# Optimization experiments

Hardware: AMD Instinct MI355X
Metric: run time of the kernel (lower is better)

The kernel has to match this reference:

```python
import jax, jax.numpy as jnp
import numpy as np

N_HEAD = 16
MASK_NEG = 1e10  # matches torch's -10000000000.0 * (1 - b)


def setup_inputs() -> dict:
    key = jax.random.key(0)
    ks = jax.random.split(key, 9)
    B, S, D = 2, 2048, 2048
    std = 0.02
    inp = {
        "x": jax.random.normal(ks[0], (B, S, D), dtype=jnp.float32),
        "Wq": jax.random.normal(ks[1], (D, D), dtype=jnp.float32) * std,
        "bq": jnp.zeros((D,), dtype=jnp.float32),
        "Wk": jax.random.normal(ks[2], (D, D), dtype=jnp.float32) * std,
        "bk": jnp.zeros((D,), dtype=jnp.float32),
        "Wv": jax.random.normal(ks[3], (D, D), dtype=jnp.float32) * std,
        "bv": jnp.zeros((D,), dtype=jnp.float32),
        "Wd": jax.random.normal(ks[4], (D, D), dtype=jnp.float32) * std,
        "bd": jnp.zeros((D,), dtype=jnp.float32),
    }
    return inp


def reference(x, Wq, bq, Wk, bk, Wv, bv, Wd, bd):
    # x: [B, S, D]; layer_past=None, query=None path (full causal prefill)
    B, S, D = x.shape
    H = N_HEAD
    hd = D // H

    def split(h):  # [B,S,D] -> [B,H,S,hd]
        return h.reshape(B, S, H, hd).transpose(0, 2, 1, 3)

    q = split(x @ Wq + bq)
    k = split(x @ Wk + bk)
    v = split(x @ Wv + bv)

    # scores [B,H,S,S]; scale=True divides by sqrt(head_dim)
    w = jnp.einsum("bhqd,bhkd->bhqk", q, k) / jnp.sqrt(jnp.float32(hd))
    b = jnp.tril(jnp.ones((S, S), dtype=w.dtype))  # causal bias buffer slice
    w = w * b - MASK_NEG * (1.0 - b)
    w = jax.nn.softmax(w, axis=-1)
    a = jnp.einsum("bhqk,bhkd->bhqd", w, v)

    a = a.transpose(0, 2, 1, 3).reshape(B, S, D)  # merge_heads
    a = a @ Wd + bd
    present = jnp.stack((k, v))  # [2, B, H, S, hd]
    return a, present
```

## Files before the change

### kernel.cpp

```cpp
#include <hip/hip_runtime.h>


typedef unsigned short ushort_t;
typedef __attribute__((ext_vector_type(8))) short short8;
typedef __attribute__((ext_vector_type(4))) float f32x4;

#define MFMA16x16x32 __builtin_amdgcn_mfma_f32_16x16x32_bf16
#define S_LEN   2048
#define DMODEL  2048
#define A_ELEMS 8388608
#define W_ELEMS 4194304

__device__ __forceinline__ ushort_t f2bf(float x) {
  unsigned u = __float_as_uint(x);
  u += 0x7FFFu + ((u >> 16) & 1u);
  return (ushort_t)(u >> 16);
}
__device__ __forceinline__ unsigned pack2(float lo, float hi) {
  return (unsigned)f2bf(lo) | ((unsigned)f2bf(hi) << 16);
}
struct f8 { float v[8]; };
__device__ __forceinline__ f8 ld8f(const float* p) {
  f8 r;
  float4 a = *(const float4*)p, b = *(const float4*)(p + 4);
  r.v[0]=a.x; r.v[1]=a.y; r.v[2]=a.z; r.v[3]=a.w;
  r.v[4]=b.x; r.v[5]=b.y; r.v[6]=b.z; r.v[7]=b.w;
  return r;
}
__device__ __forceinline__ uint4 cvt8(const f8& f) {
  uint4 o;
  o.x = pack2(f.v[0], f.v[1]); o.y = pack2(f.v[2], f.v[3]);
  o.z = pack2(f.v[4], f.v[5]); o.w = pack2(f.v[6], f.v[7]);
  return o;
}

typedef const __attribute__((address_space(1))) void* gas_t;
typedef __attribute__((address_space(3))) void* las_t;
__device__ __forceinline__ void gld16(const void* g, void* l) {
  __builtin_amdgcn_global_load_lds((gas_t)(unsigned long long)g,
                                   (las_t)(unsigned)(unsigned long long)l,
                                   16, 0, 0);
}

__global__ void __launch_bounds__(256) conv_x(const float* __restrict__ x,
                                              ushort_t* __restrict__ xb) {
  const int i = (blockIdx.x * 256 + threadIdx.x) * 8;
  f8 v = ld8f(x + i);
  *(uint4*)&xb[i] = cvt8(v);
}

__global__ void __launch_bounds__(256) trans_w(
    const float* __restrict__ w0, const float* __restrict__ w1,
    const float* __restrict__ w2, const float* __restrict__ w3,
    ushort_t* __restrict__ o0, ushort_t* __restrict__ o1,
    ushort_t* __restrict__ o2, ushort_t* __restrict__ o3) {
  __shared__ float t[64][65];
  const float* src; ushort_t* dst;
  switch (blockIdx.z) {
    case 0: src = w0; dst = o0; break;
    case 1: src = w1; dst = o1; break;
    case 2: src = w2; dst = o2; break;
    default: src = w3; dst = o3; break;
  }
  const int kb = blockIdx.y * 64, nb = blockIdx.x * 64;
  const int r = threadIdx.x >> 3, c8 = (threadIdx.x & 7) * 8;
#pragma unroll
  for (int i = 0; i < 64; i += 32) {
    *(float4*)&t[r + i][c8]     = *(const float4*)&src[(size_t)(kb + r + i) * DMODEL + nb + c8];
    *(float4*)&t[r + i][c8 + 4] = *(const float4*)&src[(size_t)(kb + r + i) * DMODEL + nb + c8 + 4];
  }
  __syncthreads();
#pragma unroll
  for (int i = 0; i < 64; i += 32) {
    float tmp[8];
#pragma unroll
    for (int j = 0; j < 8; ++j) tmp[j] = t[c8 + j][r + i];
    uint4 o;
    o.x = pack2(tmp[0], tmp[1]); o.y = pack2(tmp[2], tmp[3]);
    o.z = pack2(tmp[4], tmp[5]); o.w = pack2(tmp[6], tmp[7]);
    *(uint4*)&dst[(size_t)(nb + r + i) * DMODEL + kb + c8] = o;
  }
}

__device__ __forceinline__ void gemm_core(
    const ushort_t* __restrict__ gA, const ushort_t* __restrict__ gB,
    ushort_t* As, ushort_t* Bs, int w, int lane, int wr, int wc,
    f32x4 acc[4][4]) {
  const int sr = lane >> 2, sc = (lane & 3) * 8;
  const int l15 = lane & 15, quad = lane >> 4;
  const ushort_t* pA = gA + sc;
  const ushort_t* pB = gB + sc;
  for (int kt = 0; kt < 2048; kt += 32) {
    __syncthreads();
#pragma unroll
    for (int i = 0; i < 4; ++i) {
      const int c = i * 4 + w;
      if (c < 8)
        gld16(pA + (size_t)(c * 16 + sr) * 2048 + kt, (void*)(As + c * 512));
      else
        gld16(pB + (size_t)((c - 8) * 16 + sr) * 2048 + kt,
              (void*)(Bs + (c - 8) * 512));
    }
    __syncthreads();
    short8 af[4], bf[4];
#pragma unroll
    for (int mi = 0; mi < 4; ++mi)
      af[mi] = *(const short8*)&As[(wr + mi * 16 + l15) * 32 + quad * 8];
#pragma unroll
    for (int ni = 0; ni < 4; ++ni)
      bf[ni] = *(const short8*)&Bs[(wc + ni * 16 + l15) * 32 + quad * 8];
#pragma unroll
    for (int mi = 0; mi < 4; ++mi)
#pragma unroll
      for (int ni = 0; ni < 4; ++ni)
        acc[mi][ni] = MFMA16x16x32(af[mi], bf[ni], acc[mi][ni], 0, 0, 0);
  }
}

__global__ void __launch_bounds__(256) gemm_qkv(
    const ushort_t* __restrict__ xb,
    const ushort_t* __restrict__ wtq, const ushort_t* __restrict__ wtk,
    const ushort_t* __restrict__ wtv,
    const float* __restrict__ bq, const float* __restrict__ bk,
    const float* __restrict__ bv,
    ushort_t* __restrict__ qout, float* __restrict__ kout,
    float* __restrict__ vout) {
  __shared__ ushort_t As[4096], Bs[4096];
  const int tid = threadIdx.x, w = tid >> 6, lane = tid & 63;
  const int l15 = lane & 15, quad = lane >> 4;
  const int bx = blockIdx.x, wid = bx >> 9, r = bx & 511;
  const int tm = r & 31, tn = r >> 5;
  const int wr = (w >> 1) * 64, wc = (w & 1) * 64;
  const ushort_t* Wt = wid == 0 ? wtq : (wid == 1 ? wtk : wtv);
  const float* bias = wid == 0 ? bq : (wid == 1 ? bk : bv);

  f32x4 acc[4][4] = {};
  gemm_core(xb + (size_t)(tm * 128) * 2048, Wt + (size_t)(tn * 128) * 2048,
            As, Bs, w, lane, wr, wc, acc);

  const int row0 = tm * 128 + wr, col0 = tn * 128 + wc;
#pragma unroll
  for (int ni = 0; ni < 4; ++ni) {
    const int col = col0 + ni * 16 + l15;
    const float bv_ = bias[col];
    const int h = col >> 7, d = col & 127;
#pragma unroll
    for (int mi = 0; mi < 4; ++mi) {
#pragma unroll
      for (int j = 0; j < 4; ++j) {
        const int row = row0 + mi * 16 + quad * 4 + j;
        const int b = row >> 11, s = row & 2047;
        const size_t idx = (size_t)(((b * 16 + h) * 2048 + s)) * 128 + d;
        const float v = acc[mi][ni][j] + bv_;
        if (wid == 0) qout[idx] = f2bf(v);
        else if (wid == 1) kout[idx] = v;
        else vout[idx] = v;
      }
    }
  }
}

__global__ void __launch_bounds__(256) gemm_proj(
    const ushort_t* __restrict__ A, const ushort_t* __restrict__ Wt,
    const float* __restrict__ bias, float* __restrict__ C) {
  __shared__ ushort_t As[4096], Bs[4096];
  const int tid = threadIdx.x, w = tid >> 6, lane = tid & 63;
  const int l15 = lane & 15, quad = lane >> 4;
  const int tm = blockIdx.x & 31, tn = blockIdx.x >> 5;
  const int wr = (w >> 1) * 64, wc = (w & 1) * 64;

  f32x4 acc[4][4] = {};
  gemm_core(A + (size_t)(tm * 128) * 2048, Wt + (size_t)(tn * 128) * 2048,
            As, Bs, w, lane, wr, wc, acc);

  const int row0 = tm * 128 + wr, col0 = tn * 128 + wc;
#pragma unroll
  for (int ni = 0; ni < 4; ++ni) {
    const int col = col0 + ni * 16 + l15;
    const float bv_ = bias[col];
#pragma unroll
    for (int mi = 0; mi < 4; ++mi)
#pragma unroll
      for (int j = 0; j < 4; ++j) {
        const int row = row0 + mi * 16 + quad * 4 + j;
        C[(size_t)row * DMODEL + col] = acc[mi][ni][j] + bv_;
      }
  }
}

__global__ void __launch_bounds__(256) attn_fwd(
    const ushort_t* __restrict__ Q, const float* __restrict__ Kx,
    const float* __restrict__ Vx, ushort_t* __restrict__ O) {
  __shared__ ushort_t Ks[128 * 136];
  __shared__ ushort_t Vs[128 * 72];
  const int tid = threadIdx.x;
  const int w = tid >> 6, lane = tid & 63;
  const int l15 = lane & 15, quad = lane >> 4;
  const int bh = blockIdx.x & 31, pr = blockIdx.x >> 5;
  const int b = bh >> 4, h = bh & 15;
  const size_t base = (size_t)bh * (S_LEN * 128);
  const float cs = 0.08838834764831845f * 1.4426950408889634f;

  const int kr = tid >> 1, kc0 = (tid & 1) * 64;
  const int vk = (tid & 31) * 2, vo = (tid >> 5) * 16;

  for (int seg = 0; seg < 2; ++seg) {
    const int qt = (seg == 0) ? (15 - pr) : pr;
    const int q0 = qt * 128 + w * 32;

    short8 qf[2][4];
#pragma unroll
    for (int mi = 0; mi < 2; ++mi)
#pragma unroll
      for (int ks = 0; ks < 4; ++ks)
        qf[mi][ks] = *(const short8*)&Q[base +
            (size_t)(q0 + mi * 16 + l15) * 128 + ks * 32 + quad * 8];

    f32x4 oacc[2][8] = {};
    float mrun[2][4], lrun[2][4];
#pragma unroll
    for (int mi = 0; mi < 2; ++mi)
#pragma unroll
      for (int j = 0; j < 4; ++j) { mrun[mi][j] = -1e30f; lrun[mi][j] = 0.f; }

    for (int kt = 0; kt <= qt; ++kt) {
      const int kb = kt * 128;
      __syncthreads();
#pragma unroll
      for (int j = 0; j < 8; ++j) {
        f8 kk = ld8f(&Kx[base + (size_t)(kb + kr) * 128 + kc0 + j * 8]);
        *(uint4*)&Ks[kr * 136 + kc0 + j * 8] = cvt8(kk);
      }
      {
        f8 a0 = ld8f(&Vx[base + (size_t)(kb + vk) * 128 + vo]);
        f8 a1 = ld8f(&Vx[base + (size_t)(kb + vk) * 128 + vo + 8]);
        f8 b0 = ld8f(&Vx[base + (size_t)(kb + vk + 1) * 128 + vo]);
        f8 b1 = ld8f(&Vx[base + (size_t)(kb + vk + 1) * 128 + vo + 8]);
#pragma unroll
        for (int j = 0; j < 8; ++j) {
          *(unsigned*)&Vs[(vo + j) * 72 + vk]     = pack2(a0.v[j], b0.v[j]);
          *(unsigned*)&Vs[(vo + 8 + j) * 72 + vk] = pack2(a1.v[j], b1.v[j]);
        }
      }
      __syncthreads();

      f32x4 sacc[2][8] = {};
#pragma unroll
      for (int ks = 0; ks < 4; ++ks) {
        short8 kf[8];
#pragma unroll
        for (int ni = 0; ni < 8; ++ni)
          kf[ni] = *(const short8*)&Ks[(ni * 16 + l15) * 136 + ks * 32 + quad * 8];
#pragma unroll
        for (int mi = 0; mi < 2; ++mi)
#pragma unroll
          for (int ni = 0; ni < 8; ++ni)
            sacc[mi][ni] = MFMA16x16x32(qf[mi][ks], kf[ni], sacc[mi][ni], 0, 0, 0);
      }
      __syncthreads();

#pragma unroll
      for (int mi = 0; mi < 2; ++mi) {
#pragma unroll
        for (int j = 0; j < 4; ++j) {
          const int rl = mi * 16 + quad * 4 + j;
          const int rowg = q0 + rl;
          float t0[8];
#pragma unroll
          for (int ni = 0; ni < 8; ++ni) {
            const int kg = kb + ni * 16 + l15;
            const float s = sacc[mi][ni][j] * cs;
            t0[ni] = (kg <= rowg) ? s : -1e30f;
          }
          float rm = t0[0];
#pragma unroll
          for (int ni = 1; ni < 8; ++ni) rm = fmaxf(rm, t0[ni]);
          rm = fmaxf(rm, __shfl_xor(rm, 1));
          rm = fmaxf(rm, __shfl_xor(rm, 2));
          rm = fmaxf(rm, __shfl_xor(rm, 4));
          rm = fmaxf(rm, __shfl_xor(rm, 8));
          const float mold = mrun[mi][j];
          const float mnew = fmaxf(mold, rm);
          const float alpha = __builtin_amdgcn_exp2f(mold - mnew);
          float rs = 0.f;
#pragma unroll
          for (int ni = 0; ni < 8; ++ni) {
            const float pe = __builtin_amdgcn_exp2f(t0[ni] - mnew);
            rs += pe;
            Ks[(w * 32 + rl) * 136 + ni * 16 + l15] = f2bf(pe);
          }
          rs += __shfl_xor(rs, 1);
          rs += __shfl_xor(rs, 2);
          rs += __shfl_xor(rs, 4);
          rs += __shfl_xor(rs, 8);
          lrun[mi][j] = lrun[mi][j] * alpha + rs;
          mrun[mi][j] = mnew;
#pragma unroll
          for (int oi = 0; oi < 8; ++oi) oacc[mi][oi][j] *= alpha;
        }
      }

#pragma unroll
      for (int hh = 0; hh < 2; ++hh) {
        if (hh == 1) {
          __syncthreads();
          f8 a0 = ld8f(&Vx[base + (size_t)(kb + 64 + vk) * 128 + vo]);
          f8 a1 = ld8f(&Vx[base + (size_t)(kb + 64 + vk) * 128 + vo + 8]);
          f8 b0 = ld8f(&Vx[base + (size_t)(kb + 64 + vk + 1) * 128 + vo]);
          f8 b1 = ld8f(&Vx[base + (size_t)(kb + 64 + vk + 1) * 128 + vo + 8]);
#pragma unroll
          for (int j = 0; j < 8; ++j) {
            *(unsigned*)&Vs[(vo + j) * 72 + vk]     = pack2(a0.v[j], b0.v[j]);
            *(unsigned*)&Vs[(vo + 8 + j) * 72 + vk] = pack2(a1.v[j], b1.v[j]);
          }
          __syncthreads();
        }
#pragma unroll
        for (int ks = 0; ks < 2; ++ks) {
          short8 pf[2], vf[8];
#pragma unroll
          for (int mi = 0; mi < 2; ++mi)
            pf[mi] = *(const short8*)&Ks[(w * 32 + mi * 16 + l15) * 136 +
                                         hh * 64 + ks * 32 + quad * 8];
#pragma unroll
          for (int oi = 0; oi < 8; ++oi)
            vf[oi] = *(const short8*)&Vs[(oi * 16 + l15) * 72 + ks * 32 + quad * 8];
#pragma unroll
          for (int mi = 0; mi < 2; ++mi)
#pragma unroll
            for (int oi = 0; oi < 8; ++oi)
              oacc[mi][oi] = MFMA16x16x32(pf[mi], vf[oi], oacc[mi][oi], 0, 0, 0);
        }
      }
    }

#pragma unroll
    for (int mi = 0; mi < 2; ++mi) {
      float inv[4];
#pragma unroll
      for (int j = 0; j < 4; ++j) inv[j] = 1.f / lrun[mi][j];
#pragma unroll
      for (int oi = 0; oi < 8; ++oi) {
        const int oc = oi * 16 + l15;
#pragma unroll
        for (int j = 0; j < 4; ++j) {
          const int s = q0 + mi * 16 + quad * 4 + j;
          O[((size_t)(b * S_LEN + s)) * DMODEL + h * 128 + oc] =
              f2bf(oacc[mi][oi][j] * inv[j]);
        }
      }
    }
  }
}

extern "C" void kernel_launch(void* const* d_in, const int* in_sizes, int n_in,
                              void* d_out, int out_size, void* d_ws,
                              size_t ws_size, hipStream_t stream) {
  const float* x  = (const float*)d_in[0];
  const float* Wq = (const float*)d_in[1];
  const float* bq = (const float*)d_in[2];
  const float* Wk = (const float*)d_in[3];
  const float* bk = (const float*)d_in[4];
  const float* Wv = (const float*)d_in[5];
  const float* bv = (const float*)d_in[6];
  const float* Wd = (const float*)d_in[7];
  const float* bd = (const float*)d_in[8];

  float* out   = (float*)d_out;
  float* a_out = out;
  float* k_out = out + A_ELEMS;
  float* v_out = out + 2 * A_ELEMS;
  ushort_t* ob  = (ushort_t*)d_out;
  ushort_t* xb   = ob;
  ushort_t* q_ws = ob + A_ELEMS;

  ushort_t* ws  = (ushort_t*)d_ws;
  ushort_t* wtq = ws;
  ushort_t* wtk = ws + W_ELEMS;
  ushort_t* wtv = ws + 2 * (size_t)W_ELEMS;
  ushort_t* wtd = ws + 3 * (size_t)W_ELEMS;
  ushort_t* attn_ws = ws + 4 * (size_t)W_ELEMS;

  conv_x<<<4096, 256, 0, stream>>>(x, xb);
  trans_w<<<dim3(32, 32, 4), 256, 0, stream>>>(Wq, Wk, Wv, Wd,
                                               wtq, wtk, wtv, wtd);
  gemm_qkv<<<1536, 256, 0, stream>>>(xb, wtq, wtk, wtv, bq, bk, bv,
                                     q_ws, k_out, v_out);
  attn_fwd<<<256, 256, 0, stream>>>(q_ws, k_out, v_out, attn_ws);
  gemm_proj<<<512, 256, 0, stream>>>(attn_ws, wtd, bd, a_out);
}
```

Before: 523.7 us.

## Pre-convert K/V to bf16 with transposed V and async swizzled LDS loads in attention

The QKV GEMM now also writes a bf16 copy of K, and a new kernel transposes V into a bf16 [d][s] layout. The attention kernel loads both tiles straight into XOR-swizzled shared memory with direct global-to-LDS loads, replacing the per-tile fp32-to-bf16 conversion and the scalar V transpose. It also moves to 512 threads, with each wave owning 16 query rows, and loads the whole V tile at once instead of in two halves. This removes conversion work and extra syncs inside the inner loop, at the cost of an extra kernel, more workspace, and extra global writes for the bf16 K and transposed V copies.

```diff
diff --git a/kernel.cpp b/kernel.cpp
--- a/kernel.cpp
+++ b/kernel.cpp
@@ -82,6 +82,32 @@
   }
 }
 
+__global__ void __launch_bounds__(256) trans_v(const float* __restrict__ v,
+                                               ushort_t* __restrict__ vt) {
+  __shared__ float t[64][65];
+  const int bh = blockIdx.z;
+  const int sb = blockIdx.x * 64, db = blockIdx.y * 64;
+  const float* src = v + (size_t)bh * S_LEN * 128;
+  ushort_t* dst = vt + (size_t)bh * 128 * S_LEN;
+  const int r = threadIdx.x >> 3, c8 = (threadIdx.x & 7) * 8;
+#pragma unroll
+  for (int i = 0; i < 64; i += 32) {
+    *(float4*)&t[r + i][c8]     = *(const float4*)&src[(size_t)(sb + r + i) * 128 + db + c8];
+    *(float4*)&t[r + i][c8 + 4] = *(const float4*)&src[(size_t)(sb + r + i) * 128 + db + c8 + 4];
+  }
+  __syncthreads();
+#pragma unroll
+  for (int i = 0; i < 64; i += 32) {
+    float tmp[8];
+#pragma unroll
+    for (int j = 0; j < 8; ++j) tmp[j] = t[c8 + j][r + i];
+    uint4 o;
+    o.x = pack2(tmp[0], tmp[1]); o.y = pack2(tmp[2], tmp[3]);
+    o.z = pack2(tmp[4], tmp[5]); o.w = pack2(tmp[6], tmp[7]);
+    *(uint4*)&dst[(size_t)(db + r + i) * S_LEN + sb + c8] = o;
+  }
+}
+
 __device__ __forceinline__ void gemm_core(
     const ushort_t* __restrict__ gA, const ushort_t* __restrict__ gB,
     ushort_t* As, ushort_t* Bs, int w, int lane, int wr, int wc,
@@ -124,7 +150,7 @@
     const float* __restrict__ bq, const float* __restrict__ bk,
     const float* __restrict__ bv,
     ushort_t* __restrict__ qout, float* __restrict__ kout,
-    float* __restrict__ vout) {
+    float* __restrict__ vout, ushort_t* __restrict__ kb16) {
   __shared__ ushort_t As[4096], Bs[4096];
   const int tid = threadIdx.x, w = tid >> 6, lane = tid & 63;
   const int l15 = lane & 15, quad = lane >> 4;
@@ -153,7 +179,7 @@
         const size_t idx = (size_t)(((b * 16 + h) * 2048 + s)) * 128 + d;
         const float v = acc[mi][ni][j] + bv_;
         if (wid == 0) qout[idx] = f2bf(v);
-        else if (wid == 1) kout[idx] = v;
+        else if (wid == 1) { kout[idx] = v; kb16[idx] = f2bf(v); }
         else vout[idx] = v;
       }
     }
@@ -188,165 +214,129 @@
   }
 }
 
-__global__ void __launch_bounds__(256) attn_fwd(
-    const ushort_t* __restrict__ Q, const float* __restrict__ Kx,
-    const float* __restrict__ Vx, ushort_t* __restrict__ O) {
-  __shared__ ushort_t Ks[128 * 136];
-  __shared__ ushort_t Vs[128 * 72];
+__global__ void __launch_bounds__(512, 2) attn_fwd(
+    const ushort_t* __restrict__ Q, const ushort_t* __restrict__ Kb,
+    const ushort_t* __restrict__ Vt, ushort_t* __restrict__ O) {
+  __shared__ ushort_t KP[128 * 136];
+  __shared__ ushort_t Vs[128 * 128];
   const int tid = threadIdx.x;
   const int w = tid >> 6, lane = tid & 63;
   const int l15 = lane & 15, quad = lane >> 4;
+  const int x7 = l15 & 7;
   const int bh = blockIdx.x & 31, pr = blockIdx.x >> 5;
   const int b = bh >> 4, h = bh & 15;
-  const size_t base = (size_t)bh * (S_LEN * 128);
+  const size_t base  = (size_t)bh * (S_LEN * 128);
+  const size_t vbase = (size_t)bh * (128 * S_LEN);
   const float cs = 0.08838834764831845f * 1.4426950408889634f;
 
-  const int kr = tid >> 1, kc0 = (tid & 1) * 64;
-  const int vk = (tid & 31) * 2, vo = (tid >> 5) * 16;
+  const int srow = lane >> 4;
+  const int schunk = lane & 15;
 
   for (int seg = 0; seg < 2; ++seg) {
     const int qt = (seg == 0) ? (15 - pr) : pr;
-    const int q0 = qt * 128 + w * 32;
-
-    short8 qf[2][4];
-#pragma unroll
-    for (int mi = 0; mi < 2; ++mi)
-#pragma unroll
-      for (int ks = 0; ks < 4; ++ks)
-        qf[mi][ks] = *(const short8*)&Q[base +
-            (size_t)(q0 + mi * 16 + l15) * 128 + ks * 32 + quad * 8];
-
-    f32x4 oacc[2][8] = {};
-    float mrun[2][4], lrun[2][4];
-#pragma unroll
-    for (int mi = 0; mi < 2; ++mi)
-#pragma unroll
-      for (int j = 0; j < 4; ++j) { mrun[mi][j] = -1e30f; lrun[mi][j] = 0.f; }
+    const int q0 = qt * 128 + w * 16;
+
+    short8 qf[4];
+#pragma unroll
+    for (int ks = 0; ks < 4; ++ks)
+      qf[ks] = *(const short8*)&Q[base + (size_t)(q0 + l15) * 128 + ks * 32 + quad * 8];
+
+    f32x4 oacc[8] = {};
+    float mrun[4], lrun[4];
+#pragma unroll
+    for (int j = 0; j < 4; ++j) { mrun[j] = -1e30f; lrun[j] = 0.f; }
 
     for (int kt = 0; kt <= qt; ++kt) {
-      const int kb = kt * 128;
+      const int kb_ = kt * 128;
       __syncthreads();
 #pragma unroll
-      for (int j = 0; j < 8; ++j) {
-        f8 kk = ld8f(&Kx[base + (size_t)(kb + kr) * 128 + kc0 + j * 8]);
-        *(uint4*)&Ks[kr * 136 + kc0 + j * 8] = cvt8(kk);
-      }
-      {
-        f8 a0 = ld8f(&Vx[base + (size_t)(kb + vk) * 128 + vo]);
-        f8 a1 = ld8f(&Vx[base + (size_t)(kb + vk) * 128 + vo + 8]);
-        f8 b0 = ld8f(&Vx[base + (size_t)(kb + vk + 1) * 128 + vo]);
-        f8 b1 = ld8f(&Vx[base + (size_t)(kb + vk + 1) * 128 + vo + 8]);
-#pragma unroll
-        for (int j = 0; j < 8; ++j) {
-          *(unsigned*)&Vs[(vo + j) * 72 + vk]     = pack2(a0.v[j], b0.v[j]);
-          *(unsigned*)&Vs[(vo + 8 + j) * 72 + vk] = pack2(a1.v[j], b1.v[j]);
+      for (int i = 0; i < 4; ++i) {
+        const int r = w * 16 + i * 4 + srow;
+        const int c = schunk ^ (r & 7);
+        gld16(Kb + base + (size_t)(kb_ + r) * 128 + c * 8,
+              (void*)(KP + (w * 16 + i * 4) * 128));
+        gld16(Vt + vbase + (size_t)r * S_LEN + kb_ + c * 8,
+              (void*)(Vs + (w * 16 + i * 4) * 128));
+      }
+      __syncthreads();
+
+      f32x4 sacc[8] = {};
+#pragma unroll
+      for (int ks = 0; ks < 4; ++ks) {
+        const int sw = ((ks * 4 + quad) ^ x7) * 8;
+        short8 kf[8];
+#pragma unroll
+        for (int ni = 0; ni < 8; ++ni)
+          kf[ni] = *(const short8*)&KP[(ni * 16 + l15) * 128 + sw];
+#pragma unroll
+        for (int ni = 0; ni < 8; ++ni)
+          sacc[ni] = MFMA16x16x32(qf[ks], kf[ni], sacc[ni], 0, 0, 0);
+      }
+      __syncthreads();
+
+#pragma unroll
+      for (int j = 0; j < 4; ++j) {
+        const int rl = quad * 4 + j;
+        const int rowg = q0 + rl;
+        float t0[8];
+#pragma unroll
+        for (int ni = 0; ni < 8; ++ni) {
+          const int kg = kb_ + ni * 16 + l15;
+          const float s = sacc[ni][j] * cs;
+          t0[ni] = (kg <= rowg) ? s : -1e30f;
         }
-      }
-      __syncthreads();
-
-      f32x4 sacc[2][8] = {};
+        float rm = fmaxf(fmaxf(fmaxf(t0[0], t0[1]), fmaxf(t0[2], t0[3])),
+                         fmaxf(fmaxf(t0[4], t0[5]), fmaxf(t0[6], t0[7])));
+        rm = fmaxf(rm, __shfl_xor(rm, 1));
+        rm = fmaxf(rm, __shfl_xor(rm, 2));
+        rm = fmaxf(rm, __shfl_xor(rm, 4));
+        rm = fmaxf(rm, __shfl_xor(rm, 8));
+        const float mold = mrun[j];
+        const float mnew = fmaxf(mold, rm);
+        const float alpha = __builtin_amdgcn_exp2f(mold - mnew);
+        float rs = 0.f;
+#pragma unroll
+        for (int ni = 0; ni < 8; ++ni) {
+          const float pe = __builtin_amdgcn_exp2f(t0[ni] - mnew);
+          rs += pe;
+          KP[(w * 16 + rl) * 136 + ni * 16 + l15] = f2bf(pe);
+        }
+        rs += __shfl_xor(rs, 1);
+        rs += __shfl_xor(rs, 2);
+        rs += __shfl_xor(rs, 4);
+        rs += __shfl_xor(rs, 8);
+        lrun[j] = lrun[j] * alpha + rs;
+        mrun[j] = mnew;
+#pragma unroll
+        for (int oi = 0; oi < 8; ++oi) oacc[oi][j] *= alpha;
+      }
+
 #pragma unroll
       for (int ks = 0; ks < 4; ++ks) {
-        short8 kf[8];
-#pragma unroll
-        for (int ni = 0; ni < 8; ++ni)
-          kf[ni] = *(const short8*)&Ks[(ni * 16 + l15) * 136 + ks * 32 + quad * 8];
-#pragma unroll
-        for (int mi = 0; mi < 2; ++mi)
-#pragma unroll
-          for (int ni = 0; ni < 8; ++ni)
-            sacc[mi][ni] = MFMA16x16x32(qf[mi][ks], kf[ni], sacc[mi][ni], 0, 0, 0);
-      }
-      __syncthreads();
-
-#pragma unroll
-      for (int mi = 0; mi < 2; ++mi) {
-#pragma unroll
-        for (int j = 0; j < 4; ++j) {
-          const int rl = mi * 16 + quad * 4 + j;
-          const int rowg = q0 + rl;
-          float t0[8];
-#pragma unroll
-          for (int ni = 0; ni < 8; ++ni) {
-            const int kg = kb + ni * 16 + l15;
-            const float s = sacc[mi][ni][j] * cs;
-            t0[ni] = (kg <= rowg) ? s : -1e30f;
-          }
-          float rm = t0[0];
-#pragma unroll
-          for (int ni = 1; ni < 8; ++ni) rm = fmaxf(rm, t0[ni]);
-          rm = fmaxf(rm, __shfl_xor(rm, 1));
-          rm = fmaxf(rm, __shfl_xor(rm, 2));
-          rm = fmaxf(rm, __shfl_xor(rm, 4));
-          rm = fmaxf(rm, __shfl_xor(rm, 8));
-          const float mold = mrun[mi][j];
-          const float mnew = fmaxf(mold, rm);
-          const float alpha = __builtin_amdgcn_exp2f(mold - mnew);
-          float rs = 0.f;
-#pragma unroll
-          for (int ni = 0; ni < 8; ++ni) {
-            const float pe = __builtin_amdgcn_exp2f(t0[ni] - mnew);
-            rs += pe;
-            Ks[(w * 32 + rl) * 136 + ni * 16 + l15] = f2bf(pe);
-          }
-          rs += __shfl_xor(rs, 1);
-          rs += __shfl_xor(rs, 2);
-          rs += __shfl_xor(rs, 4);
-          rs += __shfl_xor(rs, 8);
-          lrun[mi][j] = lrun[mi][j] * alpha + rs;
-          mrun[mi][j] = mnew;
-#pragma unroll
-          for (int oi = 0; oi < 8; ++oi) oacc[mi][oi][j] *= alpha;
-        }
-      }
-
-#pragma unroll
-      for (int hh = 0; hh < 2; ++hh) {
-        if (hh == 1) {
-          __syncthreads();
-          f8 a0 = ld8f(&Vx[base + (size_t)(kb + 64 + vk) * 128 + vo]);
-          f8 a1 = ld8f(&Vx[base + (size_t)(kb + 64 + vk) * 128 + vo + 8]);
-          f8 b0 = ld8f(&Vx[base + (size_t)(kb + 64 + vk + 1) * 128 + vo]);
-          f8 b1 = ld8f(&Vx[base + (size_t)(kb + 64 + vk + 1) * 128 + vo + 8]);
-#pragma unroll
-          for (int j = 0; j < 8; ++j) {
-            *(unsigned*)&Vs[(vo + j) * 72 + vk]     = pack2(a0.v[j], b0.v[j]);
-            *(unsigned*)&Vs[(vo + 8 + j) * 72 + vk] = pack2(a1.v[j], b1.v[j]);
-          }
-          __syncthreads();
-        }
-#pragma unroll
-        for (int ks = 0; ks < 2; ++ks) {
-          short8 pf[2], vf[8];
-#pragma unroll
-          for (int mi = 0; mi < 2; ++mi)
-            pf[mi] = *(const short8*)&Ks[(w * 32 + mi * 16 + l15) * 136 +
-                                         hh * 64 + ks * 32 + quad * 8];
-#pragma unroll
-          for (int oi = 0; oi < 8; ++oi)
-            vf[oi] = *(const short8*)&Vs[(oi * 16 + l15) * 72 + ks * 32 + quad * 8];
-#pragma unroll
-          for (int mi = 0; mi < 2; ++mi)
-#pragma unroll
-            for (int oi = 0; oi < 8; ++oi)
-              oacc[mi][oi] = MFMA16x16x32(pf[mi], vf[oi], oacc[mi][oi], 0, 0, 0);
-        }
+        const int sw = ((ks * 4 + quad) ^ x7) * 8;
+        short8 pf = *(const short8*)&KP[(w * 16 + l15) * 136 + ks * 32 + quad * 8];
+        short8 vf[8];
+#pragma unroll
+        for (int oi = 0; oi < 8; ++oi)
+          vf[oi] = *(const short8*)&Vs[(oi * 16 + l15) * 128 + sw];
+#pragma unroll
+        for (int oi = 0; oi < 8; ++oi)
+          oacc[oi] = MFMA16x16x32(pf, vf[oi], oacc[oi], 0, 0, 0);
       }
     }
 
-#pragma unroll
-    for (int mi = 0; mi < 2; ++mi) {
+    {
       float inv[4];
 #pragma unroll
-      for (int j = 0; j < 4; ++j) inv[j] = 1.f / lrun[mi][j];
+      for (int j = 0; j < 4; ++j) inv[j] = 1.f / lrun[j];
 #pragma unroll
       for (int oi = 0; oi < 8; ++oi) {
         const int oc = oi * 16 + l15;
 #pragma unroll
         for (int j = 0; j < 4; ++j) {
-          const int s = q0 + mi * 16 + quad * 4 + j;
+          const int s = q0 + quad * 4 + j;
           O[((size_t)(b * S_LEN + s)) * DMODEL + h * 128 + oc] =
-              f2bf(oacc[mi][oi][j] * inv[j]);
+              f2bf(oacc[oi][j] * inv[j]);
         }
       }
     }
@@ -380,12 +370,15 @@
   ushort_t* wtv = ws + 2 * (size_t)W_ELEMS;
   ushort_t* wtd = ws + 3 * (size_t)W_ELEMS;
   ushort_t* attn_ws = ws + 4 * (size_t)W_ELEMS;
+  ushort_t* kb_ws   = attn_ws + (size_t)A_ELEMS;
+  ushort_t* vt_ws   = attn_ws + 2 * (size_t)A_ELEMS;
 
   conv_x<<<4096, 256, 0, stream>>>(x, xb);
   trans_w<<<dim3(32, 32, 4), 256, 0, stream>>>(Wq, Wk, Wv, Wd,
                                                wtq, wtk, wtv, wtd);
   gemm_qkv<<<1536, 256, 0, stream>>>(xb, wtq, wtk, wtv, bq, bk, bv,
-                                     q_ws, k_out, v_out);
-  attn_fwd<<<256, 256, 0, stream>>>(q_ws, k_out, v_out, attn_ws);
+                                     q_ws, k_out, v_out, kb_ws);
+  trans_v<<<dim3(32, 2, 32), 256, 0, stream>>>(v_out, vt_ws);
+  attn_fwd<<<256, 512, 0, stream>>>(q_ws, kb_ws, vt_ws, attn_ws);
   gemm_proj<<<512, 256, 0, stream>>>(attn_ws, wtd, bd, a_out);
 }
```

New measurement: 455.0 us. 13.1% less time.
